# Performance work log

Hardware: AMD Instinct MI355X
Metric: run time of the kernel (lower is better)

Reference implementation:

```python
import jax, jax.numpy as jnp
import numpy as np

NUM_GRAPHS = 64

def _seg_max(vals, ids, num_segments):
    # segment max with empty segments mapped to 0 (PyG scatter-max convention)
    m = jax.ops.segment_max(vals, ids, num_segments=num_segments)
    return jnp.where(jnp.isfinite(m), m, 0.0)

def setup_inputs() -> dict:
    key = jax.random.key(0)
    ks = jax.random.split(key, 10)
    N, E, F, L, LIN, OUT = 50000, 800000, 128, 3, 256, 10
    x = jax.random.normal(ks[0], (N, F), dtype=jnp.float32)
    edge_index = jax.random.randint(ks[1], (2, E), 0, N, dtype=jnp.int64)
    batch = jnp.sort(jax.random.randint(ks[2], (N,), 0, NUM_GRAPHS, dtype=jnp.int64))
    s = 0.05
    Ws_self = jax.random.normal(ks[3], (L, F, F), dtype=jnp.float32) * s
    Ws_nei = jax.random.normal(ks[4], (L, F, F), dtype=jnp.float32) * s
    bs = jnp.zeros((L, F), dtype=jnp.float32)
    lin_W = jax.random.normal(ks[5], (F, LIN), dtype=jnp.float32) * s
    lin_b = jnp.zeros((LIN,), dtype=jnp.float32)
    out_W = jax.random.normal(ks[6], (LIN, OUT), dtype=jnp.float32) * s
    out_b = jnp.zeros((OUT,), dtype=jnp.float32)
    return {"x": x, "edge_index": edge_index, "batch": batch,
            "Ws_self": Ws_self, "Ws_nei": Ws_nei, "bs": bs,
            "lin_W": lin_W, "lin_b": lin_b, "out_W": out_W, "out_b": out_b}

def reference(x, edge_index, batch, Ws_self, Ws_nei, bs, lin_W, lin_b, out_W, out_b):
    N = x.shape[0]
    src, dst = edge_index[0], edge_index[1]
    L = Ws_self.shape[0]
    for l in range(L):  # small fixed layer count
        agg = _seg_max(x[src], dst, N)                 # [N, F] max-aggregated neighbor feats
        x = jax.nn.relu(agg @ Ws_nei[l] + x @ Ws_self[l] + bs[l])
    pooled = _seg_max(x, batch, NUM_GRAPHS)            # [G, F] global max pool
    h = pooled @ lin_W + lin_b                         # [G, LIN]
    return h @ out_W + out_b                           # [G, OUT]
```

## Files before the change

### kernel.cpp

```cpp
#include <hip/hip_runtime.h>
#include <float.h>

typedef __bf16 bf16x8 __attribute__((ext_vector_type(8)));
typedef float f32x4 __attribute__((ext_vector_type(4)));
typedef unsigned short ushort8 __attribute__((ext_vector_type(8)));
typedef _Float16 h8 __attribute__((ext_vector_type(8)));

__device__ inline unsigned short f2bh(float f) {
    unsigned int u = __float_as_uint(f);
    return (unsigned short)((u + 0x7FFFu + ((u >> 16) & 1u)) >> 16);
}
__device__ inline float bh2f(unsigned short h) {
    return __uint_as_float((unsigned int)h << 16);
}
__device__ inline h8 h8max(h8 a, h8 b) {
    h8 r;
    #pragma unroll
    for (int i = 0; i < 8; ++i) r[i] = a[i] > b[i] ? a[i] : b[i];
    return r;
}
__device__ inline h8 h8fill(_Float16 v) {
    h8 r;
    #pragma unroll
    for (int i = 0; i < 8; ++i) r[i] = v;
    return r;
}


__global__ void cvt16_kernel(const float* __restrict__ xin, _Float16* __restrict__ x16,
                             int total8, int* __restrict__ cnt, int N) {
    int i = blockIdx.x * blockDim.x + threadIdx.x;
    if (i < N) cnt[i] = 0;
    if (i >= total8) return;
    const float4* p = reinterpret_cast<const float4*>(xin + (size_t)i * 8);
    float4 a = p[0], b = p[1];
    h8 o;
    o[0] = (_Float16)a.x; o[1] = (_Float16)a.y; o[2] = (_Float16)a.z; o[3] = (_Float16)a.w;
    o[4] = (_Float16)b.x; o[5] = (_Float16)b.y; o[6] = (_Float16)b.z; o[7] = (_Float16)b.w;
    *reinterpret_cast<h8*>(x16 + (size_t)i * 8) = o;
}


__global__ void hist_kernel(const int* __restrict__ dst, int E, int* __restrict__ cnt) {
    int e = blockIdx.x * blockDim.x + threadIdx.x;
    if (e < E) atomicAdd(&cnt[dst[e]], 1);
}

__global__ __launch_bounds__(256) void bsum_kernel(const int* __restrict__ cnt, int N,
                                                   int* __restrict__ bsum) {
    __shared__ int red[256];
    int t = threadIdx.x;
    int i = blockIdx.x * 256 + t;
    red[t] = (i < N) ? cnt[i] : 0;
    __syncthreads();
    for (int off = 128; off > 0; off >>= 1) {
        if (t < off) red[t] += red[t + off];
        __syncthreads();
    }
    if (t == 0) bsum[blockIdx.x] = red[0];
}

__global__ __launch_bounds__(256) void scan_apply_kernel(const int* __restrict__ cnt, int N,
                                                         const int* __restrict__ bsum, int nb,
                                                         int* __restrict__ row_start,
                                                         int* __restrict__ bcur,
                                                         unsigned int* __restrict__ pooled) {
    __shared__ int sb[256];
    __shared__ int s[256];
    int t = threadIdx.x;
    if (blockIdx.x == 0)
        for (int k = t; k < 64 * 128; k += 256) pooled[k] = 0u;
    sb[t] = (t < nb) ? bsum[t] : 0;
    int i = blockIdx.x * 256 + t;
    int v = (i < N) ? cnt[i] : 0;
    s[t] = v;
    __syncthreads();
    for (int off = 1; off < 256; off <<= 1) {
        int u0 = (t >= off) ? sb[t - off] : 0;
        int u1 = (t >= off) ? s[t - off] : 0;
        __syncthreads();
        sb[t] += u0;
        s[t] += u1;
        __syncthreads();
    }
    int base = (blockIdx.x == 0) ? 0 : sb[blockIdx.x - 1];
    int excl = base + s[t] - v;
    if (i < N) {
        row_start[i] = excl;
        if ((i & 63) == 0) bcur[i >> 6] = excl;
        if (i == N - 1) row_start[N] = excl + v;
    }
}

#define EPB 8192

__global__ __launch_bounds__(256) void partA_kernel(const int* __restrict__ src,
                                                    const int* __restrict__ dst, int E,
                                                    int nbkt, int* __restrict__ bcur,
                                                    unsigned int* __restrict__ pk) {
    __shared__ int lh[1024];
    __shared__ int lbase[1024];
    int t = threadIdx.x;
    int e0 = blockIdx.x * EPB;
    int e1 = e0 + EPB; if (e1 > E) e1 = E;
    for (int b = t; b < nbkt; b += 256) lh[b] = 0;
    __syncthreads();
    for (int e = e0 + t; e < e1; e += 256)
        atomicAdd(&lh[dst[e] >> 6], 1);
    __syncthreads();
    for (int b = t; b < nbkt; b += 256) {
        int c = lh[b];
        lbase[b] = (c > 0) ? atomicAdd(&bcur[b], c) : 0;
        lh[b] = 0;
    }
    __syncthreads();
    for (int e = e0 + t; e < e1; e += 256) {
        int d = dst[e];
        int b = d >> 6;
        int r = atomicAdd(&lh[b], 1);
        pk[lbase[b] + r] = ((unsigned int)src[e] << 6) | (unsigned int)(d & 63);
    }
}

__global__ __launch_bounds__(256) void partB_kernel(const unsigned int* __restrict__ pk,
                                                    const int* __restrict__ row_start,
                                                    int N, int E, int* __restrict__ col) {
    __shared__ int lrs[64];
    __shared__ int lcur[64];
    int b = blockIdx.x;
    int base = b * 64;
    int t = threadIdx.x;
    if (t < 64) {
        int node = base + t;
        lrs[t] = (node < N) ? row_start[node] : E;
        lcur[t] = 0;
    }
    __syncthreads();
    int lo = row_start[base];
    int nxt = base + 64; if (nxt > N) nxt = N;
    int hi = row_start[nxt];
    for (int i = lo + t; i < hi; i += 256) {
        unsigned int w = pk[i];
        int dl = w & 63u;
        int s = (int)(w >> 6);
        int r = atomicAdd(&lcur[dl], 1);
        col[lrs[dl] + r] = s;
    }
}


__global__ void wprep_kernel(const float* __restrict__ Wn, const float* __restrict__ Wsf,
                             int total, unsigned short* __restrict__ Wfh,
                             unsigned short* __restrict__ Wfl) {
    int idx = blockIdx.x * blockDim.x + threadIdx.x;
    if (idx >= total) return;
    int c = idx & 127;
    int k = (idx >> 7) & 127;
    int p = (idx >> 14) & 1;
    int l = idx >> 15;
    const float* W = p ? Wsf : Wn;
    float v = W[(size_t)l * 16384 + k * 128 + c];
    unsigned short hi = f2bh(v);
    unsigned short lo = f2bh(v - bh2f(hi));
    size_t d = ((((size_t)l * 2 + p) * 16 + (k >> 3)) * 128 + c) * 8 + (k & 7);
    Wfh[d] = hi;
    Wfl[d] = lo;
}


__global__ __launch_bounds__(256) void fused_layer(
    const _Float16* __restrict__ xin16,
    const int* __restrict__ row_start, const int* __restrict__ col,
    const unsigned short* __restrict__ Wfh, const unsigned short* __restrict__ Wfl,
    const float* __restrict__ bias, _Float16* __restrict__ xout16, int N)
{
    __shared__ _Float16 lds[2 * 32 * 136];
    const int tid = threadIdx.x;
    const int row0 = blockIdx.x * 32;

    {
        const int g = tid >> 4;
        const int l16 = tid & 15;
        const _Float16* xb = xin16 + (size_t)l16 * 8;
        #pragma unroll
        for (int pass = 0; pass < 2; ++pass) {
            int nl = pass * 16 + g;
            int node = row0 + nl;
            const _Float16 NEG = (_Float16)(-65504.0f);
            h8 a0 = h8fill(NEG), a1 = a0, a2 = a0, a3 = a0;
            int deg = 0;
            if (node < N) {
                int beg = row_start[node];
                deg = row_start[node + 1] - beg;
                int j = 0;
                for (; j + 4 <= deg; j += 4) {
                    int s0 = col[beg + j];
                    int s1 = col[beg + j + 1];
                    int s2 = col[beg + j + 2];
                    int s3 = col[beg + j + 3];
                    a0 = h8max(a0, *reinterpret_cast<const h8*>(xb + (size_t)s0 * 128));
                    a1 = h8max(a1, *reinterpret_cast<const h8*>(xb + (size_t)s1 * 128));
                    a2 = h8max(a2, *reinterpret_cast<const h8*>(xb + (size_t)s2 * 128));
                    a3 = h8max(a3, *reinterpret_cast<const h8*>(xb + (size_t)s3 * 128));
                }
                for (; j < deg; ++j) {
                    int s0 = col[beg + j];
                    a0 = h8max(a0, *reinterpret_cast<const h8*>(xb + (size_t)s0 * 128));
                }
            }
            a0 = h8max(h8max(a0, a1), h8max(a2, a3));
            if (deg == 0) a0 = h8fill((_Float16)0.f);
            *reinterpret_cast<h8*>(&lds[nl * 136 + l16 * 8]) = a0;
        }
    }
    #pragma unroll
    for (int it = 0; it < 2; ++it) {
        int idx = tid + it * 256;
        int r = idx >> 4;
        int c = idx & 15;
        int grow = row0 + r;
        h8 v = h8fill((_Float16)0.f);
        if (grow < N) v = *reinterpret_cast<const h8*>(&xin16[(size_t)grow * 128 + c * 8]);
        *reinterpret_cast<h8*>(&lds[4352 + r * 136 + c * 8]) = v;
    }
    __syncthreads();

    const int lane = tid & 63;
    const int wid  = tid >> 6;
    const int l15  = lane & 15;
    const int lg   = lane >> 4;
    const int ch   = wid & 1;
    const int rg   = wid >> 1;

    f32x4 acc[4];
    #pragma unroll
    for (int nt = 0; nt < 4; ++nt) { f32x4 z = {0.f, 0.f, 0.f, 0.f}; acc[nt] = z; }

    #pragma unroll
    for (int p = 0; p < 2; ++p) {
        const _Float16* arow = lds + p * 4352 + (rg * 16 + l15) * 136 + lg * 8;
        const unsigned short* wh0 = Wfh + p * 16384 + (size_t)(ch * 64 + l15) * 8 + lg * 1024;
        const unsigned short* wl0 = Wfl + p * 16384 + (size_t)(ch * 64 + l15) * 8 + lg * 1024;
        #pragma unroll
        for (int ks = 0; ks < 4; ++ks) {
            h8 av = *reinterpret_cast<const h8*>(arow + ks * 32);
            ushort8 hh, ll;
            #pragma unroll
            for (int j = 0; j < 8; ++j) {
                float f = (float)av[j];
                unsigned short hi = f2bh(f);
                float r = f - bh2f(hi);
                hh[j] = hi;
                ll[j] = (unsigned short)(__float_as_uint(r) >> 16);
            }
            bf16x8 ah = __builtin_bit_cast(bf16x8, hh);
            bf16x8 al = __builtin_bit_cast(bf16x8, ll);
            const unsigned short* whk = wh0 + ks * 4096;
            const unsigned short* wlk = wl0 + ks * 4096;
            #pragma unroll
            for (int nt = 0; nt < 4; ++nt) {
                bf16x8 bh = *reinterpret_cast<const bf16x8*>(whk + nt * 128);
                bf16x8 bl = *reinterpret_cast<const bf16x8*>(wlk + nt * 128);
                acc[nt] = __builtin_amdgcn_mfma_f32_16x16x32_bf16(ah, bh, acc[nt], 0, 0, 0);
                acc[nt] = __builtin_amdgcn_mfma_f32_16x16x32_bf16(al, bh, acc[nt], 0, 0, 0);
                acc[nt] = __builtin_amdgcn_mfma_f32_16x16x32_bf16(ah, bl, acc[nt], 0, 0, 0);
            }
        }
    }

    #pragma unroll
    for (int nt = 0; nt < 4; ++nt) {
        int colb = ch * 64 + nt * 16 + l15;
        float bv = bias[colb];
        #pragma unroll
        for (int rr = 0; rr < 4; ++rr) {
            int row = row0 + rg * 16 + lg * 4 + rr;
            if (row < N) {
                float o = fmaxf(acc[nt][rr] + bv, 0.f);
                xout16[(size_t)row * 128 + colb] = (_Float16)o;
            }
        }
    }
}


#define POOL_CHUNK 128

__global__ __launch_bounds__(128) void pool_kernel(const _Float16* __restrict__ x16,
                                                   const int* __restrict__ batch,
                                                   int N,
                                                   unsigned int* __restrict__ pooled) {
    int f = threadIdx.x;
    int n0 = blockIdx.x * POOL_CHUNK;
    if (n0 >= N) return;
    int n1 = n0 + POOL_CHUNK; if (n1 > N) n1 = N;
    int g = batch[n0];
    float m = 0.f;
    for (int n = n0; n < n1; ++n) {
        int bg = batch[n];
        if (bg != g) {
            atomicMax(&pooled[g * 128 + f], __float_as_uint(m));
            m = 0.f; g = bg;
        }
        m = fmaxf(m, (float)x16[(size_t)n * 128 + f]);
    }
    atomicMax(&pooled[g * 128 + f], __float_as_uint(m));
}


__global__ __launch_bounds__(256) void head_kernel(
    const float* __restrict__ pooled,
    const float* __restrict__ linW, const float* __restrict__ linb,
    const float* __restrict__ outW, const float* __restrict__ outb,
    float* __restrict__ out)
{
    __shared__ float pl[128];
    __shared__ float hrow[256];
    int g = blockIdx.x, t = threadIdx.x;
    if (t < 128) pl[t] = pooled[g * 128 + t];
    __syncthreads();
    float acc = linb[t];
    for (int k = 0; k < 128; ++k) acc += pl[k] * linW[k * 256 + t];
    hrow[t] = acc;
    __syncthreads();
    if (t < 10) {
        float o = outb[t];
        for (int k = 0; k < 256; ++k) o += hrow[k] * outW[k * 10 + t];
        out[g * 10 + t] = o;
    }
}


static inline size_t align_up(size_t v, size_t a) { return (v + a - 1) & ~(a - 1); }

extern "C" void kernel_launch(void* const* d_in, const int* in_sizes, int n_in,
                              void* d_out, int out_size, void* d_ws, size_t ws_size,
                              hipStream_t stream) {
    const float* x      = (const float*)d_in[0];
    const int*   ei     = (const int*)d_in[1];
    const int*   batch  = (const int*)d_in[2];
    const float* WsSelf = (const float*)d_in[3];
    const float* WsNei  = (const float*)d_in[4];
    const float* bsAll  = (const float*)d_in[5];
    const float* linW   = (const float*)d_in[6];
    const float* linb   = (const float*)d_in[7];
    const float* outW   = (const float*)d_in[8];
    const float* outb   = (const float*)d_in[9];

    const int N = in_sizes[0] / 128;
    const int E = in_sizes[1] / 2;
    const int L = in_sizes[3] / (128 * 128);
    const int* src = ei;
    const int* dst = ei + E;
    const int nb2 = (N + 63) / 64;

    char* w = (char*)d_ws;
    int* cnt       = (int*)w;  w += align_up((size_t)N * 4, 256);
    int* row_start = (int*)w;  w += align_up((size_t)(N + 1) * 4, 256);
    int* bcur      = (int*)w;  w += align_up((size_t)nb2 * 4, 256);
    int* bsum      = (int*)w;  w += align_up(256 * 4, 256);
    unsigned int* pk = (unsigned int*)w; w += align_up((size_t)E * 4, 256);
    int* col       = (int*)w;  w += align_up((size_t)E * 4, 256);
    _Float16* x16in = (_Float16*)w; w += align_up((size_t)N * 128 * 2, 256);
    _Float16* xa16  = (_Float16*)w; w += align_up((size_t)N * 128 * 2, 256);
    _Float16* xb16  = (_Float16*)w; w += align_up((size_t)N * 128 * 2, 256);
    float* pooled  = (float*)w; w += align_up((size_t)64 * 128 * 4, 256);
    unsigned short* Wfh = (unsigned short*)w; w += align_up((size_t)L * 2 * 16384 * 2, 256);
    unsigned short* Wfl = (unsigned short*)w; w += align_up((size_t)L * 2 * 16384 * 2, 256);
    (void)ws_size;

    cvt16_kernel<<<(N * 16 + 255) / 256, 256, 0, stream>>>(x, x16in, N * 16, cnt, N);

    const int wtotal = L * 2 * 128 * 128;
    wprep_kernel<<<(wtotal + 255) / 256, 256, 0, stream>>>(WsNei, WsSelf, wtotal, Wfh, Wfl);

    const int nb = (N + 255) / 256;
    hist_kernel<<<(E + 255) / 256, 256, 0, stream>>>(dst, E, cnt);
    bsum_kernel<<<nb, 256, 0, stream>>>(cnt, N, bsum);
    scan_apply_kernel<<<nb, 256, 0, stream>>>(cnt, N, bsum, nb, row_start, bcur,
                                              (unsigned int*)pooled);
    partA_kernel<<<(E + EPB - 1) / EPB, 256, 0, stream>>>(src, dst, E, nb2, bcur, pk);
    partB_kernel<<<nb2, 256, 0, stream>>>(pk, row_start, N, E, col);

    const _Float16* xin16 = x16in;
    _Float16* bufs[2] = { xa16, xb16 };
    for (int l = 0; l < L; ++l) {
        fused_layer<<<(N + 31) / 32, 256, 0, stream>>>(
            xin16, row_start, col,
            Wfh + (size_t)l * 2 * 16384, Wfl + (size_t)l * 2 * 16384,
            bsAll + (size_t)l * 128, bufs[l & 1], N);
        xin16 = bufs[l & 1];
    }

    pool_kernel<<<(N + POOL_CHUNK - 1) / POOL_CHUNK, 128, 0, stream>>>(
        xin16, batch, N, (unsigned int*)pooled);
    head_kernel<<<64, 256, 0, stream>>>(pooled, linW, linb, outW, outb, (float*)d_out);
}
```

Measured before the change: 309.8 us.

## Split fused layer into separate gather-max aggregation and MFMA GEMM kernels

Unfuses the per-layer kernel. A standalone agg_kernel does the neighbor max-gather with one node per 16 threads and an 8-way unrolled accumulator, writing an fp16 aggregate buffer. A slimmer layer_mfma kernel reads the aggregate and self features directly from global memory with no LDS staging or barrier. The aim is higher occupancy and more loads in flight for the latency-bound gather, at the cost of an extra N×128 fp16 write and read per layer plus one more launch per layer.

```diff
diff --git a/kernel.cpp b/kernel.cpp
--- a/kernel.cpp
+++ b/kernel.cpp
@@ -146,6 +146,49 @@
         int r = atomicAdd(&lcur[dl], 1);
         col[lrs[dl] + r] = s;
     }
+}
+
+
+__global__ __launch_bounds__(256) void agg_kernel(const _Float16* __restrict__ x16,
+                                                  const int* __restrict__ row_start,
+                                                  const int* __restrict__ col,
+                                                  _Float16* __restrict__ agg16, int N) {
+    int gid = blockIdx.x * blockDim.x + threadIdx.x;
+    int node = gid >> 4;
+    int l16 = gid & 15;
+    if (node >= N) return;
+    int beg = row_start[node];
+    int deg = row_start[node + 1] - beg;
+    const _Float16* xb = x16 + (size_t)l16 * 8;
+    const _Float16 NEG = (_Float16)(-65504.0f);
+    h8 a0 = h8fill(NEG), a1 = a0, a2 = a0, a3 = a0, a4 = a0, a5 = a0, a6 = a0, a7 = a0;
+    int j = 0;
+    for (; j + 8 <= deg; j += 8) {
+        int s0 = col[beg + j];
+        int s1 = col[beg + j + 1];
+        int s2 = col[beg + j + 2];
+        int s3 = col[beg + j + 3];
+        int s4 = col[beg + j + 4];
+        int s5 = col[beg + j + 5];
+        int s6 = col[beg + j + 6];
+        int s7 = col[beg + j + 7];
+        a0 = h8max(a0, *reinterpret_cast<const h8*>(xb + (size_t)s0 * 128));
+        a1 = h8max(a1, *reinterpret_cast<const h8*>(xb + (size_t)s1 * 128));
+        a2 = h8max(a2, *reinterpret_cast<const h8*>(xb + (size_t)s2 * 128));
+        a3 = h8max(a3, *reinterpret_cast<const h8*>(xb + (size_t)s3 * 128));
+        a4 = h8max(a4, *reinterpret_cast<const h8*>(xb + (size_t)s4 * 128));
+        a5 = h8max(a5, *reinterpret_cast<const h8*>(xb + (size_t)s5 * 128));
+        a6 = h8max(a6, *reinterpret_cast<const h8*>(xb + (size_t)s6 * 128));
+        a7 = h8max(a7, *reinterpret_cast<const h8*>(xb + (size_t)s7 * 128));
+    }
+    for (; j < deg; ++j) {
+        int s0 = col[beg + j];
+        a0 = h8max(a0, *reinterpret_cast<const h8*>(xb + (size_t)s0 * 128));
+    }
+    a0 = h8max(h8max(h8max(a0, a1), h8max(a2, a3)),
+               h8max(h8max(a4, a5), h8max(a6, a7)));
+    if (deg == 0) a0 = h8fill((_Float16)0.f);
+    *reinterpret_cast<h8*>(&agg16[(size_t)node * 128 + l16 * 8]) = a0;
 }
 
 
@@ -168,82 +211,34 @@
 }
 
 
-__global__ __launch_bounds__(256) void fused_layer(
-    const _Float16* __restrict__ xin16,
-    const int* __restrict__ row_start, const int* __restrict__ col,
+__global__ __launch_bounds__(256) void layer_mfma(
+    const _Float16* __restrict__ agg16, const _Float16* __restrict__ xin16,
     const unsigned short* __restrict__ Wfh, const unsigned short* __restrict__ Wfl,
     const float* __restrict__ bias, _Float16* __restrict__ xout16, int N)
 {
-    __shared__ _Float16 lds[2 * 32 * 136];
-    const int tid = threadIdx.x;
-    const int row0 = blockIdx.x * 32;
-
-    {
-        const int g = tid >> 4;
-        const int l16 = tid & 15;
-        const _Float16* xb = xin16 + (size_t)l16 * 8;
-        #pragma unroll
-        for (int pass = 0; pass < 2; ++pass) {
-            int nl = pass * 16 + g;
-            int node = row0 + nl;
-            const _Float16 NEG = (_Float16)(-65504.0f);
-            h8 a0 = h8fill(NEG), a1 = a0, a2 = a0, a3 = a0;
-            int deg = 0;
-            if (node < N) {
-                int beg = row_start[node];
-                deg = row_start[node + 1] - beg;
-                int j = 0;
-                for (; j + 4 <= deg; j += 4) {
-                    int s0 = col[beg + j];
-                    int s1 = col[beg + j + 1];
-                    int s2 = col[beg + j + 2];
-                    int s3 = col[beg + j + 3];
-                    a0 = h8max(a0, *reinterpret_cast<const h8*>(xb + (size_t)s0 * 128));
-                    a1 = h8max(a1, *reinterpret_cast<const h8*>(xb + (size_t)s1 * 128));
-                    a2 = h8max(a2, *reinterpret_cast<const h8*>(xb + (size_t)s2 * 128));
-                    a3 = h8max(a3, *reinterpret_cast<const h8*>(xb + (size_t)s3 * 128));
-                }
-                for (; j < deg; ++j) {
-                    int s0 = col[beg + j];
-                    a0 = h8max(a0, *reinterpret_cast<const h8*>(xb + (size_t)s0 * 128));
-                }
-            }
-            a0 = h8max(h8max(a0, a1), h8max(a2, a3));
-            if (deg == 0) a0 = h8fill((_Float16)0.f);
-            *reinterpret_cast<h8*>(&lds[nl * 136 + l16 * 8]) = a0;
-        }
-    }
-    #pragma unroll
-    for (int it = 0; it < 2; ++it) {
-        int idx = tid + it * 256;
-        int r = idx >> 4;
-        int c = idx & 15;
-        int grow = row0 + r;
-        h8 v = h8fill((_Float16)0.f);
-        if (grow < N) v = *reinterpret_cast<const h8*>(&xin16[(size_t)grow * 128 + c * 8]);
-        *reinterpret_cast<h8*>(&lds[4352 + r * 136 + c * 8]) = v;
-    }
-    __syncthreads();
-
-    const int lane = tid & 63;
-    const int wid  = tid >> 6;
+    const int lane = threadIdx.x & 63;
+    const int wid  = threadIdx.x >> 6;
     const int l15  = lane & 15;
     const int lg   = lane >> 4;
     const int ch   = wid & 1;
     const int rg   = wid >> 1;
+    const int row0 = blockIdx.x * 32 + rg * 16;
 
     f32x4 acc[4];
     #pragma unroll
     for (int nt = 0; nt < 4; ++nt) { f32x4 z = {0.f, 0.f, 0.f, 0.f}; acc[nt] = z; }
 
+    int rc = row0 + l15; if (rc > N - 1) rc = N - 1;
+
     #pragma unroll
     for (int p = 0; p < 2; ++p) {
-        const _Float16* arow = lds + p * 4352 + (rg * 16 + l15) * 136 + lg * 8;
+        const _Float16* A = p ? xin16 : agg16;
+        const _Float16* a = A + (size_t)rc * 128 + lg * 8;
         const unsigned short* wh0 = Wfh + p * 16384 + (size_t)(ch * 64 + l15) * 8 + lg * 1024;
         const unsigned short* wl0 = Wfl + p * 16384 + (size_t)(ch * 64 + l15) * 8 + lg * 1024;
         #pragma unroll
         for (int ks = 0; ks < 4; ++ks) {
-            h8 av = *reinterpret_cast<const h8*>(arow + ks * 32);
+            h8 av = *reinterpret_cast<const h8*>(a + ks * 32);
             ushort8 hh, ll;
             #pragma unroll
             for (int j = 0; j < 8; ++j) {
@@ -274,7 +269,7 @@
         float bv = bias[colb];
         #pragma unroll
         for (int rr = 0; rr < 4; ++rr) {
-            int row = row0 + rg * 16 + lg * 4 + rr;
+            int row = row0 + lg * 4 + rr;
             if (row < N) {
                 float o = fmaxf(acc[nt][rr] + bv, 0.f);
                 xout16[(size_t)row * 128 + colb] = (_Float16)o;
@@ -361,6 +356,7 @@
     int* bsum      = (int*)w;  w += align_up(256 * 4, 256);
     unsigned int* pk = (unsigned int*)w; w += align_up((size_t)E * 4, 256);
     int* col       = (int*)w;  w += align_up((size_t)E * 4, 256);
+    _Float16* agg16 = (_Float16*)w; w += align_up((size_t)N * 128 * 2, 256);
     _Float16* x16in = (_Float16*)w; w += align_up((size_t)N * 128 * 2, 256);
     _Float16* xa16  = (_Float16*)w; w += align_up((size_t)N * 128 * 2, 256);
     _Float16* xb16  = (_Float16*)w; w += align_up((size_t)N * 128 * 2, 256);
@@ -385,8 +381,9 @@
     const _Float16* xin16 = x16in;
     _Float16* bufs[2] = { xa16, xb16 };
     for (int l = 0; l < L; ++l) {
-        fused_layer<<<(N + 31) / 32, 256, 0, stream>>>(
-            xin16, row_start, col,
+        agg_kernel<<<(N * 16 + 255) / 256, 256, 0, stream>>>(xin16, row_start, col, agg16, N);
+        layer_mfma<<<(N + 31) / 32, 256, 0, stream>>>(
+            agg16, xin16,
             Wfh + (size_t)l * 2 * 16384, Wfl + (size_t)l * 2 * 16384,
             bsAll + (size_t)l * 128, bufs[l & 1], N);
         xin16 = bufs[l & 1];
```

New measurement: 325.4 us. +5.0%, slower.
